# Kernel optimization log

Hardware: AMD Instinct MI355X
Metric: run time of the kernel (lower is better)

Reference implementation:

```python
import jax, jax.numpy as jnp
import numpy as np

NHEAD = 16

def setup_inputs() -> dict:
    key = jax.random.key(0)
    ks = jax.random.split(key, 5)
    B, S, D = 4, 2048, 1024
    x = jax.random.normal(ks[0], (B, S, D), dtype=jnp.float32)
    in_proj_weight = jax.random.normal(ks[1], (3 * D, D), dtype=jnp.float32) * (D ** -0.5)
    in_proj_bias = jax.random.normal(ks[2], (3 * D,), dtype=jnp.float32) * 0.02
    out_w = jax.random.normal(ks[3], (D, D), dtype=jnp.float32) * (D ** -0.5)
    out_b = jax.random.normal(ks[4], (D,), dtype=jnp.float32) * 0.02
    return {"x": x, "in_proj_weight": in_proj_weight, "in_proj_bias": in_proj_bias,
            "out_w": out_w, "out_b": out_b}

def reference(x, in_proj_weight, in_proj_bias, out_w, out_b):
    # Faithful to nn.MultiheadAttention self-attn (prefill path, no mask).
    B, S, D = x.shape
    H = NHEAD
    hd = D // H
    qkv = x @ in_proj_weight.T + in_proj_bias            # [B,S,3D]
    q, k, v = jnp.split(qkv, 3, axis=-1)                 # each [B,S,D]
    def heads(t):
        return t.reshape(B, S, H, hd).transpose(0, 2, 1, 3)  # [B,H,S,hd]
    q, k, v = heads(q), heads(k), heads(v)
    scale = hd ** -0.5
    scores = jnp.einsum('bhqd,bhkd->bhqk', q * scale, k)  # [B,H,S,S]
    attn = jax.nn.softmax(scores, axis=-1)
    o = jnp.einsum('bhqk,bhkd->bhqd', attn, v)            # [B,H,S,hd]
    o = o.transpose(0, 2, 1, 3).reshape(B, S, D)
    return o @ out_w.T + out_b
```

## Files before the change

### kernel.cpp

```cpp
#include <hip/hip_runtime.h>
#include <hip/hip_bf16.h>
#include <math.h>

typedef __bf16 bf16_t;
typedef __bf16 bf16x8 __attribute__((ext_vector_type(8)));
typedef float  f32x4  __attribute__((ext_vector_type(4)));

#define DEV __device__ __forceinline__

#define BSZ    4
#define SEQ    2048
#define DMODEL 1024
#define NHEADS 16
#define HDIM   64
#define MROWS  (BSZ*SEQ)
#define KDIM   1024
#define NQKV   (3*DMODEL)

#define GLOAD_LDS16(src, dst)                                                  \
  __builtin_amdgcn_global_load_lds(                                            \
      (__attribute__((address_space(1))) void*)(void*)(src),                   \
      (__attribute__((address_space(3))) void*)(dst), 16, 0, 0)

DEV unsigned cvtpk_bf16(float lo, float hi) {
  unsigned r;
  asm("v_cvt_pk_bf16_f32 %0, %1, %2" : "=v"(r) : "v"(lo), "v"(hi));
  return r;
}

__global__ void cast_f32_to_bf16(const float* __restrict__ in,
                                 bf16_t* __restrict__ out, int n4) {
  union U { bf16_t b[4]; uint2 u; };
  for (int i = blockIdx.x * blockDim.x + threadIdx.x; i < n4;
       i += gridDim.x * blockDim.x) {
    float4 v = reinterpret_cast<const float4*>(in)[i];
    U r;
    r.b[0] = (bf16_t)v.x; r.b[1] = (bf16_t)v.y;
    r.b[2] = (bf16_t)v.z; r.b[3] = (bf16_t)v.w;
    reinterpret_cast<uint2*>(out)[i] = r.u;
  }
}

DEV void gemm_tile(const bf16_t* __restrict__ A, const bf16_t* __restrict__ Bt,
                   int row0, int col0, char* smem, f32x4 acc[4][4]) {
  const int t    = threadIdx.x;
  const int lane = t & 63;
  const int wid  = t >> 6;
  const int wm   = (wid >> 1) * 64;
  const int wn   = (wid & 1) * 64;
  const int l15  = lane & 15;
  const int lhi  = lane >> 4;

  char* As = smem;
  char* Bs = smem + 16384;

  const f32x4 fzero = {0.f, 0.f, 0.f, 0.f};
#pragma unroll
  for (int mi = 0; mi < 4; mi++)
#pragma unroll
    for (int ni = 0; ni < 4; ni++) acc[mi][ni] = fzero;

  const char* Abase = (const char*)A;
  const char* Bbase = (const char*)Bt;

  for (int k0 = 0; k0 < KDIM; k0 += 64) {
    __syncthreads();
#pragma unroll
    for (int i = 0; i < 4; i++) {
      int o   = (t + i * 256) * 16;
      int row = o >> 7;
      int cbs = (o & 127) ^ ((row & 7) << 4);
      GLOAD_LDS16(Abase + ((size_t)(row0 + row) * KDIM + k0) * 2 + cbs, As + o);
      GLOAD_LDS16(Bbase + ((size_t)(col0 + row) * KDIM + k0) * 2 + cbs, Bs + o);
    }
    __syncthreads();

#pragma unroll
    for (int ks = 0; ks < 2; ks++) {
      bf16x8 a[4], b[4];
      int byt = ks * 64 + lhi * 16;
#pragma unroll
      for (int mi = 0; mi < 4; mi++) {
        int r = wm + mi * 16 + l15;
        a[mi] = *(const bf16x8*)(As + r * 128 + (byt ^ ((r & 7) << 4)));
      }
#pragma unroll
      for (int ni = 0; ni < 4; ni++) {
        int r = wn + ni * 16 + l15;
        b[ni] = *(const bf16x8*)(Bs + r * 128 + (byt ^ ((r & 7) << 4)));
      }
#pragma unroll
      for (int mi = 0; mi < 4; mi++)
#pragma unroll
        for (int ni = 0; ni < 4; ni++)
          acc[mi][ni] = __builtin_amdgcn_mfma_f32_16x16x32_bf16(
              a[mi], b[ni], acc[mi][ni], 0, 0, 0);
    }
  }
}

__global__ void gemm_qkv_kernel(const bf16_t* __restrict__ xb,
                                const bf16_t* __restrict__ wqkv,
                                const float* __restrict__ bias,
                                bf16_t* __restrict__ Qg, bf16_t* __restrict__ Kg,
                                bf16_t* __restrict__ Vt) {
  __shared__ char smem[32768];
  f32x4 acc[4][4];
  const int bx = blockIdx.x;
  const int wg = (bx & 7) * 192 + (bx >> 3);
  const int mt = wg / 24, nt = wg % 24;
  const int row0 = mt * 128, col0 = nt * 128;
  gemm_tile(xb, wqkv, row0, col0, smem, acc);

  const int t = threadIdx.x, lane = t & 63, wid = t >> 6;
  const int wm = (wid >> 1) * 64, wn = (wid & 1) * 64;
  const int l15 = lane & 15, lhi = lane >> 4;
  const float qscale = 0.125f * 1.44269504f;
#pragma unroll
  for (int mi = 0; mi < 4; mi++)
#pragma unroll
    for (int ni = 0; ni < 4; ni++)
#pragma unroll
      for (int j = 0; j < 4; j++) {
        int m = row0 + wm + mi * 16 + lhi * 4 + j;
        int n = col0 + wn + ni * 16 + l15;
        float v = acc[mi][ni][j] + bias[n];
        int b = m >> 11, s = m & 2047;
        int which = n >> 10, rem = n & 1023;
        int h = rem >> 6, d = rem & 63;
        size_t bh = (size_t)(b * NHEADS + h);
        if (which == 0) {
          Qg[(bh * SEQ + s) * HDIM + d] = (bf16_t)(v * qscale);
        } else if (which == 1) {
          Kg[(bh * SEQ + s) * HDIM + d] = (bf16_t)v;
        } else {
          int sp = (s & ~63) + 4 * (s & 15) + ((s >> 4) & 3);
          Vt[(bh * HDIM + d) * SEQ + sp] = (bf16_t)v;
        }
      }
}

__global__ void gemm_out_kernel(const bf16_t* __restrict__ Og,
                                const bf16_t* __restrict__ wo,
                                const float* __restrict__ bias,
                                float* __restrict__ out) {
  __shared__ char smem[32768];
  f32x4 acc[4][4];
  const int bx = blockIdx.x;
  const int wg = (bx & 7) * 64 + (bx >> 3);
  const int mt = wg >> 3, nt = wg & 7;
  const int row0 = mt * 128, col0 = nt * 128;
  gemm_tile(Og, wo, row0, col0, smem, acc);

  const int t = threadIdx.x, lane = t & 63, wid = t >> 6;
  const int wm = (wid >> 1) * 64, wn = (wid & 1) * 64;
  const int l15 = lane & 15, lhi = lane >> 4;
#pragma unroll
  for (int mi = 0; mi < 4; mi++)
#pragma unroll
    for (int ni = 0; ni < 4; ni++)
#pragma unroll
      for (int j = 0; j < 4; j++) {
        int m = row0 + wm + mi * 16 + lhi * 4 + j;
        int n = col0 + wn + ni * 16 + l15;
        out[(size_t)m * DMODEL + n] = acc[mi][ni][j] + bias[n];
      }
}

__global__ __launch_bounds__(512, 4)
void attn_kernel(const bf16_t* __restrict__ Qg,
                 const bf16_t* __restrict__ Kg,
                 const bf16_t* __restrict__ Vt,
                 bf16_t* __restrict__ Og) {
  __shared__ char smem[65536];
  char* Ps = smem + 32768;

  const int t = threadIdx.x, lane = t & 63, w = t >> 6;
  const int l15 = lane & 15, lhi = lane >> 4;
  char* Pw = Ps + w * 4096;

  const int xcd = blockIdx.x & 7, slot = blockIdx.x >> 3;
  const int bh = xcd * 8 + (slot >> 3), qt = slot & 7;

  const char* Kb = (const char*)Kg + (size_t)bh * SEQ * HDIM * 2;
  const char* Vb = (const char*)Vt + (size_t)bh * HDIM * SEQ * 2;

  auto STAGE = [&](int buf, int kt) {
    char* Kd = smem + buf * 16384;
    char* Vd = Kd + 8192;
    int o   = t * 16;
    int row = o >> 7;
    int cbs = (o & 127) ^ ((row & 7) << 4);
    GLOAD_LDS16(Kb + (size_t)(kt * 64 + row) * 128 + cbs, Kd + o);
    GLOAD_LDS16(Vb + (size_t)row * 4096 + kt * 128 + cbs, Vd + o);
  };

  STAGE(1, 0);

  bf16x8 qf[2][2];
#pragma unroll
  for (int mi = 0; mi < 2; mi++)
#pragma unroll
    for (int ks = 0; ks < 2; ks++) {
      int q = qt * 256 + w * 32 + mi * 16 + l15;
      qf[mi][ks] = *(const bf16x8*)((const char*)Qg +
                   ((size_t)bh * SEQ + q) * 128 + ks * 64 + lhi * 16);
    }

  const f32x4 fzero = {0.f, 0.f, 0.f, 0.f};
  float lpart[2][4];
  f32x4 oacc[2][4];
#pragma unroll
  for (int mi = 0; mi < 2; mi++)
#pragma unroll
    for (int j = 0; j < 4; j++) { lpart[mi][j] = 0.f; oacc[mi][j] = fzero; }

  int cur = 1;
  for (int kt = 0; kt < SEQ / 64; kt++) {
    __syncthreads();
    if (kt < SEQ / 64 - 1) STAGE(cur ^ 1, kt + 1);

    char* Ks = smem + cur * 16384;
    char* Vs = Ks + 8192;

    f32x4 sacc[2][4];
#pragma unroll
    for (int mi = 0; mi < 2; mi++)
#pragma unroll
      for (int ni = 0; ni < 4; ni++) sacc[mi][ni] = fzero;
    __builtin_amdgcn_s_setprio(1);
#pragma unroll
    for (int ks = 0; ks < 2; ks++) {
      bf16x8 kf[4];
      int byt = ks * 64 + lhi * 16;
#pragma unroll
      for (int ni = 0; ni < 4; ni++) {
        int r = ni * 16 + l15;
        kf[ni] = *(const bf16x8*)(Ks + r * 128 + (byt ^ ((r & 7) << 4)));
      }
#pragma unroll
      for (int mi = 0; mi < 2; mi++)
#pragma unroll
        for (int ni = 0; ni < 4; ni++)
          sacc[mi][ni] = __builtin_amdgcn_mfma_f32_16x16x32_bf16(
              qf[mi][ks], kf[ni], sacc[mi][ni], 0, 0, 0);
    }
    __builtin_amdgcn_s_setprio(0);

#pragma unroll
    for (int mi = 0; mi < 2; mi++)
#pragma unroll
      for (int j = 0; j < 4; j++) {
        float p[4];
#pragma unroll
        for (int ni = 0; ni < 4; ni++)
          p[ni] = __builtin_amdgcn_exp2f(sacc[mi][ni][j]);
        lpart[mi][j] += (p[0] + p[1]) + (p[2] + p[3]);
        int rl = mi * 16 + lhi * 4 + j;
        uint2 pk;
        pk.x = cvtpk_bf16(p[0], p[1]);
        pk.y = cvtpk_bf16(p[2], p[3]);
        *(uint2*)(Pw + rl * 128 + ((8 * l15) ^ ((rl & 7) << 4))) = pk;
      }

    __builtin_amdgcn_s_setprio(1);
#pragma unroll
    for (int ks = 0; ks < 2; ks++) {
      bf16x8 pf[2], vf[4];
      int byt = ks * 64 + lhi * 16;
#pragma unroll
      for (int mi = 0; mi < 2; mi++) {
        int rl = mi * 16 + l15;
        pf[mi] = *(const bf16x8*)(Pw + rl * 128 + (byt ^ ((rl & 7) << 4)));
      }
#pragma unroll
      for (int db = 0; db < 4; db++) {
        int r = db * 16 + l15;
        vf[db] = *(const bf16x8*)(Vs + r * 128 + (byt ^ ((r & 7) << 4)));
      }
#pragma unroll
      for (int mi = 0; mi < 2; mi++)
#pragma unroll
        for (int db = 0; db < 4; db++)
          oacc[mi][db] = __builtin_amdgcn_mfma_f32_16x16x32_bf16(
              pf[mi], vf[db], oacc[mi][db], 0, 0, 0);
    }
    __builtin_amdgcn_s_setprio(0);
    cur ^= 1;
  }

  float linv[2][4];
#pragma unroll
  for (int mi = 0; mi < 2; mi++)
#pragma unroll
    for (int j = 0; j < 4; j++) {
      float ls = lpart[mi][j];
      ls += __shfl_xor(ls, 1, 64);
      ls += __shfl_xor(ls, 2, 64);
      ls += __shfl_xor(ls, 4, 64);
      ls += __shfl_xor(ls, 8, 64);
      linv[mi][j] = 1.0f / ls;
    }
  const int b = bh >> 4, h = bh & 15;
#pragma unroll
  for (int mi = 0; mi < 2; mi++)
#pragma unroll
    for (int db = 0; db < 4; db++)
#pragma unroll
      for (int j = 0; j < 4; j++) {
        int srow = qt * 256 + w * 32 + mi * 16 + lhi * 4 + j;
        int d = db * 16 + l15;
        float v = oacc[mi][db][j] * linv[mi][j];
        Og[((size_t)b * SEQ + srow) * DMODEL + h * HDIM + d] = (bf16_t)v;
      }
}

extern "C" void kernel_launch(void* const* d_in, const int* in_sizes, int n_in,
                              void* d_out, int out_size, void* d_ws,
                              size_t ws_size, hipStream_t stream) {
  (void)in_sizes; (void)n_in; (void)out_size; (void)ws_size;
  const float* x     = (const float*)d_in[0];
  const float* w_in  = (const float*)d_in[1];
  const float* b_in  = (const float*)d_in[2];
  const float* w_out = (const float*)d_in[3];
  const float* b_out = (const float*)d_in[4];
  float* out = (float*)d_out;

  char* ws = (char*)d_ws;
  bf16_t* xb  = (bf16_t*)ws; ws += (size_t)MROWS * KDIM * 2;
  bf16_t* wqb = (bf16_t*)ws; ws += (size_t)NQKV * KDIM * 2;
  bf16_t* wob = (bf16_t*)ws; ws += (size_t)DMODEL * KDIM * 2;
  bf16_t* Qg  = (bf16_t*)ws; ws += (size_t)MROWS * DMODEL * 2;
  bf16_t* Kg  = (bf16_t*)ws; ws += (size_t)MROWS * DMODEL * 2;
  bf16_t* Vt  = (bf16_t*)ws; ws += (size_t)MROWS * DMODEL * 2;
  bf16_t* Og  = (bf16_t*)ws; ws += (size_t)MROWS * DMODEL * 2;

  cast_f32_to_bf16<<<2048, 256, 0, stream>>>(x, xb, MROWS * KDIM / 4);
  cast_f32_to_bf16<<<1024, 256, 0, stream>>>(w_in, wqb, NQKV * KDIM / 4);
  cast_f32_to_bf16<<<512, 256, 0, stream>>>(w_out, wob, DMODEL * KDIM / 4);

  gemm_qkv_kernel<<<64 * 24, 256, 0, stream>>>(xb, wqb, b_in, Qg, Kg, Vt);
  attn_kernel<<<512, 512, 0, stream>>>(Qg, Kg, Vt, Og);
  gemm_out_kernel<<<64 * 8, 256, 0, stream>>>(Og, wob, b_out, out);
}
```

Before: 186.1 us.

## Stage V transpose through LDS for coalesced stores; precompute attention LDS offsets

In the QKV GEMM epilogue, tiles that produce V now write bias-added bf16 values into shared memory, then repack them into 16-byte vector stores along the sequence axis of the transposed V layout. Previously each element was a scattered 2-byte global store. Q/K tiles keep the old per-element path but drop the V branch. Separately, the attention kernel hoists the swizzled LDS offsets and global staging pointers out of the inner loop so per-iteration address arithmetic shrinks. The cost is a slightly larger shared allocation and two extra barriers in the V epilogue.

```diff
diff --git a/kernel.cpp b/kernel.cpp
--- a/kernel.cpp
+++ b/kernel.cpp
@@ -104,7 +104,7 @@
                                 const float* __restrict__ bias,
                                 bf16_t* __restrict__ Qg, bf16_t* __restrict__ Kg,
                                 bf16_t* __restrict__ Vt) {
-  __shared__ char smem[32768];
+  __shared__ char smem[34816];
   f32x4 acc[4][4];
   const int bx = blockIdx.x;
   const int wg = (bx & 7) * 192 + (bx >> 3);
@@ -116,28 +116,65 @@
   const int wm = (wid >> 1) * 64, wn = (wid & 1) * 64;
   const int l15 = lane & 15, lhi = lane >> 4;
   const float qscale = 0.125f * 1.44269504f;
-#pragma unroll
-  for (int mi = 0; mi < 4; mi++)
-#pragma unroll
-    for (int ni = 0; ni < 4; ni++)
-#pragma unroll
-      for (int j = 0; j < 4; j++) {
-        int m = row0 + wm + mi * 16 + lhi * 4 + j;
-        int n = col0 + wn + ni * 16 + l15;
-        float v = acc[mi][ni][j] + bias[n];
-        int b = m >> 11, s = m & 2047;
-        int which = n >> 10, rem = n & 1023;
-        int h = rem >> 6, d = rem & 63;
-        size_t bh = (size_t)(b * NHEADS + h);
-        if (which == 0) {
-          Qg[(bh * SEQ + s) * HDIM + d] = (bf16_t)(v * qscale);
-        } else if (which == 1) {
-          Kg[(bh * SEQ + s) * HDIM + d] = (bf16_t)v;
-        } else {
-          int sp = (s & ~63) + 4 * (s & 15) + ((s >> 4) & 3);
-          Vt[(bh * HDIM + d) * SEQ + sp] = (bf16_t)v;
+
+  if (nt < 16) {
+#pragma unroll
+    for (int mi = 0; mi < 4; mi++)
+#pragma unroll
+      for (int ni = 0; ni < 4; ni++)
+#pragma unroll
+        for (int j = 0; j < 4; j++) {
+          int m = row0 + wm + mi * 16 + lhi * 4 + j;
+          int n = col0 + wn + ni * 16 + l15;
+          float v = acc[mi][ni][j] + bias[n];
+          int b = m >> 11, s = m & 2047;
+          int which = n >> 10, rem = n & 1023;
+          int h = rem >> 6, d = rem & 63;
+          size_t bh = (size_t)(b * NHEADS + h);
+          if (which == 0) {
+            Qg[(bh * SEQ + s) * HDIM + d] = (bf16_t)(v * qscale);
+          } else {
+            Kg[(bh * SEQ + s) * HDIM + d] = (bf16_t)v;
+          }
         }
-      }
+  } else {
+    __syncthreads();
+#pragma unroll
+    for (int mi = 0; mi < 4; mi++)
+#pragma unroll
+      for (int ni = 0; ni < 4; ni++) {
+        int nl = wn + ni * 16 + l15;
+        int n  = col0 + nl;
+        float bi = bias[n];
+        int mbase = wm + mi * 16 + lhi * 4;
+        float v0 = acc[mi][ni][0] + bi, v1 = acc[mi][ni][1] + bi;
+        float v2 = acc[mi][ni][2] + bi, v3 = acc[mi][ni][3] + bi;
+        *(unsigned*)(smem + nl * 272 + mbase * 2)     = cvtpk_bf16(v0, v1);
+        *(unsigned*)(smem + nl * 272 + mbase * 2 + 4) = cvtpk_bf16(v2, v3);
+      }
+    __syncthreads();
+    const int b  = row0 >> 11, s0 = row0 & 2047;
+    const int hbase = (col0 - 2048) >> 6;
+#pragma unroll
+    for (int it = 0; it < 8; it++) {
+      int idx = it * 256 + t;
+      int nl = idx >> 4, T = (idx >> 3) & 1, c = idx & 7;
+      const char* rb = smem + nl * 272 + T * 128 + 4 * c;
+      unsigned r0 = *(const unsigned*)(rb);
+      unsigned r1 = *(const unsigned*)(rb + 32);
+      unsigned r2 = *(const unsigned*)(rb + 64);
+      unsigned r3 = *(const unsigned*)(rb + 96);
+      uint4 o;
+      o.x = (r0 & 0xffffu) | (r1 << 16);
+      o.y = (r2 & 0xffffu) | (r3 << 16);
+      o.z = (r0 >> 16) | (r1 & 0xffff0000u);
+      o.w = (r2 >> 16) | (r3 & 0xffff0000u);
+      int h = hbase + (nl >> 6), d = nl & 63;
+      size_t elem = ((size_t)(b * NHEADS + h) * HDIM + d) * SEQ +
+                    (size_t)(s0 + T * 64 + 8 * c);
+      *(uint4*)((char*)Vt + elem * 2) = o;
+    }
+  }
 }
 
 __global__ void gemm_out_kernel(const bf16_t* __restrict__ Og,
@@ -185,14 +222,25 @@
   const char* Kb = (const char*)Kg + (size_t)bh * SEQ * HDIM * 2;
   const char* Vb = (const char*)Vt + (size_t)bh * HDIM * SEQ * 2;
 
+  const int so = t * 16;
+  const int srow = so >> 7;
+  const int scbs = (so & 127) ^ ((srow & 7) << 4);
+  const char* gK = Kb + (size_t)srow * 128 + scbs;
+  const char* gV = Vb + (size_t)srow * 4096 + scbs;
+
+  const int swz = (l15 & 7) << 4;
+  const int koff0 = l15 * 128 + ((lhi * 16) ^ swz);
+  const int koff1 = l15 * 128 + ((64 + lhi * 16) ^ swz);
+  int woff[4];
+#pragma unroll
+  for (int j = 0; j < 4; j++)
+    woff[j] = (lhi * 4 + j) * 128 + ((8 * l15) ^ (((lhi * 4 + j) & 7) << 4));
+
   auto STAGE = [&](int buf, int kt) {
     char* Kd = smem + buf * 16384;
     char* Vd = Kd + 8192;
-    int o   = t * 16;
-    int row = o >> 7;
-    int cbs = (o & 127) ^ ((row & 7) << 4);
-    GLOAD_LDS16(Kb + (size_t)(kt * 64 + row) * 128 + cbs, Kd + o);
-    GLOAD_LDS16(Vb + (size_t)row * 4096 + kt * 128 + cbs, Vd + o);
+    GLOAD_LDS16(gK + (size_t)kt * 8192, Kd + so);
+    GLOAD_LDS16(gV + (size_t)kt * 128, Vd + so);
   };
 
   STAGE(1, 0);
@@ -231,13 +279,11 @@
     __builtin_amdgcn_s_setprio(1);
 #pragma unroll
     for (int ks = 0; ks < 2; ks++) {
+      const int ko = ks ? koff1 : koff0;
       bf16x8 kf[4];
-      int byt = ks * 64 + lhi * 16;
-#pragma unroll
-      for (int ni = 0; ni < 4; ni++) {
-        int r = ni * 16 + l15;
-        kf[ni] = *(const bf16x8*)(Ks + r * 128 + (byt ^ ((r & 7) << 4)));
-      }
+#pragma unroll
+      for (int ni = 0; ni < 4; ni++)
+        kf[ni] = *(const bf16x8*)(Ks + ko + ni * 2048);
 #pragma unroll
       for (int mi = 0; mi < 2; mi++)
 #pragma unroll
@@ -256,28 +302,23 @@
         for (int ni = 0; ni < 4; ni++)
           p[ni] = __builtin_amdgcn_exp2f(sacc[mi][ni][j]);
         lpart[mi][j] += (p[0] + p[1]) + (p[2] + p[3]);
-        int rl = mi * 16 + lhi * 4 + j;
         uint2 pk;
         pk.x = cvtpk_bf16(p[0], p[1]);
         pk.y = cvtpk_bf16(p[2], p[3]);
-        *(uint2*)(Pw + rl * 128 + ((8 * l15) ^ ((rl & 7) << 4))) = pk;
+        *(uint2*)(Pw + mi * 2048 + woff[j]) = pk;
       }
 
     __builtin_amdgcn_s_setprio(1);
 #pragma unroll
     for (int ks = 0; ks < 2; ks++) {
+      const int ko = ks ? koff1 : koff0;
       bf16x8 pf[2], vf[4];
-      int byt = ks * 64 + lhi * 16;
-#pragma unroll
-      for (int mi = 0; mi < 2; mi++) {
-        int rl = mi * 16 + l15;
-        pf[mi] = *(const bf16x8*)(Pw + rl * 128 + (byt ^ ((rl & 7) << 4)));
-      }
-#pragma unroll
-      for (int db = 0; db < 4; db++) {
-        int r = db * 16 + l15;
-        vf[db] = *(const bf16x8*)(Vs + r * 128 + (byt ^ ((r & 7) << 4)));
-      }
+#pragma unroll
+      for (int mi = 0; mi < 2; mi++)
+        pf[mi] = *(const bf16x8*)(Pw + ko + mi * 2048);
+#pragma unroll
+      for (int db = 0; db < 4; db++)
+        vf[db] = *(const bf16x8*)(Vs + ko + db * 2048);
 #pragma unroll
       for (int mi = 0; mi < 2; mi++)
 #pragma unroll
```

Measured after the change: 164.4 us. 11.7% less time.
